# Kernel tuning notes

Measured on AMD Instinct MI355X. Metric: run time of the kernel, lower is better.

Reference implementation:

```python
import jax, jax.numpy as jnp
import numpy as np
from jax import lax

B, T, SDIM, ADIM, HDIM, NH, NBLK, MAXT = 4, 512, 64, 32, 512, 8, 6, 4096
DFF = 4 * HDIM
S = 3 * T  # (num_state_tokens + 1) * context_len
DH = HDIM // NH


def _layernorm(x, g, b, eps=1e-5):
    m = jnp.mean(x, axis=-1, keepdims=True)
    v = jnp.mean((x - m) ** 2, axis=-1, keepdims=True)
    return (x - m) * lax.rsqrt(v + eps) * g + b


def setup_inputs() -> dict:
    key = jax.random.key(0)
    ks = iter(jax.random.split(key, 40))

    def nrm(shape, scale=0.02):
        return jax.random.normal(next(ks), shape, jnp.float32) * scale

    inp = {
        "timesteps": jax.random.randint(next(ks), (B, T), 0, MAXT),
        "state_0": jax.random.normal(next(ks), (B, T, SDIM), jnp.float32),
        "state_1": jax.random.normal(next(ks), (B, T, SDIM), jnp.float32),
        "actions": jax.random.normal(next(ks), (B, T, ADIM), jnp.float32),
        # embeddings / input projections
        "time_emb": nrm((MAXT, HDIM)),
        "Ws": nrm((SDIM, HDIM)), "bs": jnp.zeros((HDIM,), jnp.float32),
        "Wa": nrm((ADIM, HDIM)), "ba": jnp.zeros((HDIM,), jnp.float32),
        # stacked per-block transformer params (leading axis = n_blocks)
        "Wq": nrm((NBLK, HDIM, HDIM)), "bq": jnp.zeros((NBLK, HDIM), jnp.float32),
        "Wk": nrm((NBLK, HDIM, HDIM)), "bk": jnp.zeros((NBLK, HDIM), jnp.float32),
        "Wv": nrm((NBLK, HDIM, HDIM)), "bv": jnp.zeros((NBLK, HDIM), jnp.float32),
        "Wo": nrm((NBLK, HDIM, HDIM)), "bo": jnp.zeros((NBLK, HDIM), jnp.float32),
        "W1": nrm((NBLK, HDIM, DFF)), "b1": jnp.zeros((NBLK, DFF), jnp.float32),
        "W2": nrm((NBLK, DFF, HDIM)), "b2": jnp.zeros((NBLK, HDIM), jnp.float32),
        "ln1_g": jnp.ones((NBLK, HDIM), jnp.float32), "ln1_b": jnp.zeros((NBLK, HDIM), jnp.float32),
        "ln2_g": jnp.ones((NBLK, HDIM), jnp.float32), "ln2_b": jnp.zeros((NBLK, HDIM), jnp.float32),
        # embed layernorm + action head
        "eln_g": jnp.ones((HDIM,), jnp.float32), "eln_b": jnp.zeros((HDIM,), jnp.float32),
        "Wp": nrm((HDIM, ADIM)), "bp": jnp.zeros((ADIM,), jnp.float32),
    }
    return inp


def reference(timesteps, state_0, state_1, actions, time_emb, Ws, bs, Wa, ba,
              Wq, bq, Wk, bk, Wv, bv, Wo, bo, W1, b1, W2, b2,
              ln1_g, ln1_b, ln2_g, ln2_b, eln_g, eln_b, Wp, bp):
    te = time_emb[timesteps]                       # (B, T, H)
    s0 = state_0 @ Ws + bs + te                    # shared state embedding
    s1 = state_1 @ Ws + bs + te
    ae = actions @ Wa + ba + te
    # interleave: (B, T, 3, H) -> (B, 3T, H), token order [s0, s1, a] per timestep
    h = jnp.stack([s0, s1, ae], axis=2).reshape(B, S, HDIM)
    h = _layernorm(h, eln_g, eln_b)

    causal = jnp.tril(jnp.ones((S, S), dtype=bool))
    scale = 1.0 / float(DH) ** 0.5

    def block(x, p):
        wq, bq_, wk, bk_, wv, bv_, wo, bo_, w1, b1_, w2, b2_, g1, be1, g2, be2 = p
        q = (x @ wq + bq_).reshape(B, S, NH, DH)
        k = (x @ wk + bk_).reshape(B, S, NH, DH)
        v = (x @ wv + bv_).reshape(B, S, NH, DH)
        scores = jnp.einsum('bihd,bjhd->bhij', q, k) * scale
        scores = jnp.where(causal, scores, -jnp.inf)
        attn = jax.nn.softmax(scores, axis=-1)
        ctx = jnp.einsum('bhij,bjhd->bihd', attn, v).reshape(B, S, HDIM)
        x = x + (ctx @ wo + bo_)
        x = _layernorm(x, g1, be1)
        mlp = jax.nn.gelu(x @ w1 + b1_, approximate=False) @ w2 + b2_
        x = _layernorm(x + mlp, g2, be2)
        return x, None

    h, _ = lax.scan(block, h,
                    (Wq, bq, Wk, bk, Wv, bv, Wo, bo, W1, b1, W2, b2,
                     ln1_g, ln1_b, ln2_g, ln2_b))

    h = h.reshape(B, T, 3, HDIM)                   # (B, T, num_tokens, H)
    act_in = h[:, :, 1]                            # token index -2 = last state token
    return act_in @ Wp + bp                        # (B, T, act_dim)
```

## Files before the change

kernel.cpp:

```cpp
#include <hip/hip_runtime.h>
#include <hip/hip_bf16.h>
#include <math.h>

#define BB 4
#define TT 512
#define SDIM 64
#define ADIM 32
#define HDIM 512
#define NH 8
#define NBLK 6
#define DFF 2048
#define SS 1536
#define DH 64
#define MS (BB*SS)
#define SZE ((size_t)MS * HDIM)

typedef __attribute__((ext_vector_type(8))) __bf16 bf16x8;
typedef __attribute__((ext_vector_type(4))) float f32x4;

__device__ __forceinline__ __bf16 f2b(float x) { return (__bf16)x; }

__device__ __forceinline__ void gll16(const void* g, void* l) {
    __builtin_amdgcn_global_load_lds(
        (const __attribute__((address_space(1))) unsigned int*)g,
        (__attribute__((address_space(3))) unsigned int*)l, 16, 0, 0);
}

__global__ __launch_bounds__(512) void embed_ln_kernel(
    const int* __restrict__ timesteps,
    const float* __restrict__ state0, const float* __restrict__ state1,
    const float* __restrict__ actions, const float* __restrict__ time_emb,
    const float* __restrict__ Ws, const float* __restrict__ bs,
    const float* __restrict__ Wa, const float* __restrict__ ba,
    const float* __restrict__ eg, const float* __restrict__ eb,
    __bf16* __restrict__ h_bf)
{
    __shared__ float xs[8][64];
    __shared__ float acc_s[8][512];
    __shared__ int tss[8];
    int c = blockIdx.x, t = blockIdx.y, b = blockIdx.z;
    int i0 = c * 8;
    int tid = threadIdx.x;
    int K = (t == 2) ? ADIM : SDIM;
    int ksh = (t == 2) ? 5 : 6;
    const float* W    = (t == 2) ? Wa : Ws;
    const float* bias = (t == 2) ? ba : bs;
    const float* src  = (t == 0) ? state0  + ((size_t)(b*TT + i0)) * SDIM
                      : (t == 1) ? state1  + ((size_t)(b*TT + i0)) * SDIM
                                 : actions + ((size_t)(b*TT + i0)) * ADIM;

    if (tid < 8) tss[tid] = timesteps[b*TT + i0 + tid];
    for (int idx = tid; idx < 8 * K; idx += 512) {
        int r = idx >> ksh, kk = idx & (K - 1);
        xs[r][kk] = src[r * K + kk];
    }
    __syncthreads();

    float acc[8];
    #pragma unroll
    for (int r = 0; r < 8; ++r)
        acc[r] = bias[tid] + time_emb[(size_t)tss[r] * HDIM + tid];
    for (int kk = 0; kk < K; ++kk) {
        float w = W[(size_t)kk * HDIM + tid];
        #pragma unroll
        for (int r = 0; r < 8; ++r) acc[r] += xs[r][kk] * w;
    }
    #pragma unroll
    for (int r = 0; r < 8; ++r) acc_s[r][tid] = acc[r];
    __syncthreads();

    int w = tid >> 6, lane = tid & 63;
    float4 p0 = *(const float4*)&acc_s[w][lane * 8];
    float4 p1 = *(const float4*)&acc_s[w][lane * 8 + 4];
    float v[8] = {p0.x, p0.y, p0.z, p0.w, p1.x, p1.y, p1.z, p1.w};
    float s = 0.f, sq = 0.f;
    #pragma unroll
    for (int u = 0; u < 8; ++u) { s += v[u]; sq += v[u] * v[u]; }
    #pragma unroll
    for (int off = 1; off < 64; off <<= 1) { s += __shfl_xor(s, off); sq += __shfl_xor(sq, off); }
    float mean = s * (1.f / HDIM);
    float var  = sq * (1.f / HDIM) - mean * mean;
    float inv  = rsqrtf(var + 1e-5f);
    float4 g0 = *(const float4*)(eg + lane * 8), g1 = *(const float4*)(eg + lane * 8 + 4);
    float4 b0 = *(const float4*)(eb + lane * 8), b1 = *(const float4*)(eb + lane * 8 + 4);
    float gg[8] = {g0.x, g0.y, g0.z, g0.w, g1.x, g1.y, g1.z, g1.w};
    float bbv[8] = {b0.x, b0.y, b0.z, b0.w, b1.x, b1.y, b1.z, b1.w};
    __bf16 o8[8];
    #pragma unroll
    for (int u = 0; u < 8; ++u) o8[u] = f2b((v[u] - mean) * inv * gg[u] + bbv[u]);
    int row = b * SS + (i0 + w) * 3 + t;
    *(uint4*)(h_bf + (size_t)row * HDIM + lane * 8) = *(uint4*)o8;
}

template<int NP>
__global__ __launch_bounds__(256) void ln_add_kernel(
    __bf16* __restrict__ h_bf, const __bf16* __restrict__ parts,
    const float* __restrict__ g, const float* __restrict__ bvec)
{
    int w = threadIdx.x >> 6, lane = threadIdx.x & 63;
    int row = blockIdx.x * 4 + w;
    size_t base = (size_t)row * HDIM + lane * 8;
    bf16x8 h8 = *(const bf16x8*)(h_bf + base);
    bf16x8 p8[NP];
    #pragma unroll
    for (int p = 0; p < NP; ++p) p8[p] = *(const bf16x8*)(parts + p * SZE + base);
    float v[8], s = 0.f, sq = 0.f;
    #pragma unroll
    for (int u = 0; u < 8; ++u) {
        float acc = (float)h8[u];
        #pragma unroll
        for (int p = 0; p < NP; ++p) acc += (float)p8[p][u];
        v[u] = acc;
        s += acc; sq += acc * acc;
    }
    #pragma unroll
    for (int off = 1; off < 64; off <<= 1) { s += __shfl_xor(s, off); sq += __shfl_xor(sq, off); }
    float mean = s * (1.f / HDIM);
    float var  = sq * (1.f / HDIM) - mean * mean;
    float inv  = rsqrtf(var + 1e-5f);
    float4 g0 = *(const float4*)(g + lane * 8), g1 = *(const float4*)(g + lane * 8 + 4);
    float4 b0 = *(const float4*)(bvec + lane * 8), b1 = *(const float4*)(bvec + lane * 8 + 4);
    float gg[8] = {g0.x, g0.y, g0.z, g0.w, g1.x, g1.y, g1.z, g1.w};
    float bbv[8] = {b0.x, b0.y, b0.z, b0.w, b1.x, b1.y, b1.z, b1.w};
    __bf16 o8[8];
    #pragma unroll
    for (int u = 0; u < 8; ++u) o8[u] = f2b((v[u] - mean) * inv * gg[u] + bbv[u]);
    *(uint4*)(h_bf + base) = *(uint4*)o8;
}

__global__ __launch_bounds__(256) void pack_kernel(
    const float* __restrict__ Wq, const float* __restrict__ Wk,
    const float* __restrict__ Wv, const float* __restrict__ Wo,
    const float* __restrict__ W1, const float* __restrict__ W2,
    const float* __restrict__ bq_, const float* __restrict__ bk_, const float* __restrict__ bv_,
    __bf16* __restrict__ wqkvT, __bf16* __restrict__ woT,
    __bf16* __restrict__ w1T, __bf16* __restrict__ w2T, float* __restrict__ biasq)
{
    int lyr = blockIdx.y;
    const float* wq = Wq + (size_t)lyr * HDIM * HDIM;
    const float* wk = Wk + (size_t)lyr * HDIM * HDIM;
    const float* wv = Wv + (size_t)lyr * HDIM * HDIM;
    const float* wo = Wo + (size_t)lyr * HDIM * HDIM;
    const float* w1 = W1 + (size_t)lyr * HDIM * DFF;
    const float* w2 = W2 + (size_t)lyr * DFF * HDIM;
    const float* bqL = bq_ + (size_t)lyr * HDIM;
    const float* bkL = bk_ + (size_t)lyr * HDIM;
    const float* bvL = bv_ + (size_t)lyr * HDIM;
    wqkvT += (size_t)lyr * 1536 * 512;
    woT   += (size_t)lyr * 512 * 512;
    w1T   += (size_t)lyr * 2048 * 512;
    w2T   += (size_t)lyr * 512 * 2048;
    biasq += (size_t)lyr * 1536;

    int bid = blockIdx.x;
    int tid = threadIdx.x;
    if (bid == 768) {
        for (int i = tid; i < 1536; i += 256)
            biasq[i] = (i < 512) ? bqL[i] : ((i < 1024) ? bkL[i-512] : bvL[i-1024]);
        return;
    }
    __shared__ float Ls[64][65];
    const float* src; __bf16* dst; int K, N, kt, nt;
    if (bid < 192) {
        int sec = bid / 64, t = bid % 64;
        src = (sec == 0) ? wq : (sec == 1) ? wk : wv;
        dst = wqkvT + (size_t)sec * 512 * 512;
        K = 512; N = 512; nt = t >> 3; kt = t & 7;
    } else if (bid < 256) {
        int t = bid - 192; src = wo; dst = woT; K = 512; N = 512; nt = t >> 3; kt = t & 7;
    } else if (bid < 512) {
        int t = bid - 256; src = w1; dst = w1T; K = 512; N = 2048; nt = t >> 3; kt = t & 7;
    } else {
        int t = bid - 512; src = w2; dst = w2T; K = 2048; N = 512; nt = t & 7; kt = t >> 3;
    }
    int k0 = kt * 64, n0 = nt * 64;
    int rr = tid >> 4, cc = (tid & 15) * 4;
    #pragma unroll
    for (int p = 0; p < 4; ++p) {
        float4 v = *(const float4*)(src + (size_t)(k0 + rr + p*16) * N + n0 + cc);
        Ls[rr + p*16][cc] = v.x; Ls[rr + p*16][cc+1] = v.y;
        Ls[rr + p*16][cc+2] = v.z; Ls[rr + p*16][cc+3] = v.w;
    }
    __syncthreads();
    int nn = tid >> 3, kc = (tid & 7) * 8;
    #pragma unroll
    for (int p = 0; p < 2; ++p) {
        __bf16 t8[8];
        #pragma unroll
        for (int t2 = 0; t2 < 8; ++t2) t8[t2] = f2b(Ls[kc + t2][nn + p*32]);
        *(uint4*)(dst + (size_t)(n0 + nn + p*32) * K + k0 + kc) = *(uint4*)t8;
    }
}

template<int MT, bool VTMODE>
__global__ __launch_bounds__(256) void gemm_mfma(
    const __bf16* __restrict__ A, const __bf16* __restrict__ Bt,
    const float* __restrict__ bias, __bf16* __restrict__ C,
    __bf16* __restrict__ VTout,
    int N, int Ksub, int lda, int ldb, int ldc, int gelu, size_t cSplitStride)
{
    constexpr int MI = MT / 32;
    constexpr int SMB0 = 2*MT*64 + 2*128*64;
    constexpr int SMB = (MT*132*2 > SMB0) ? MT*132*2 : SMB0;
    __shared__ __align__(16) char sm[SMB];
    __bf16* As = (__bf16*)sm;
    __bf16* Bs = (__bf16*)(sm + 2*MT*64);
    int tid = threadIdx.x;
    int wave = tid >> 6, lane = tid & 63;
    int l15 = lane & 15, quad = lane >> 4;
    int wy = wave >> 1, wx = wave & 1;
    int m0 = blockIdx.y * MT, n0 = blockIdx.x * 128;
    int zs = blockIdx.z;
    int kbase = zs * Ksub;
    C += (size_t)zs * cSplitStride;

    int srow = lane >> 2;
    int clog = (lane & 3) ^ ((lane >> 3) & 3);
    int pchunk = (quad ^ ((l15 >> 1) & 3)) * 8;

    f32x4 acc[MI][4];
    #pragma unroll
    for (int i = 0; i < MI; ++i)
        #pragma unroll
        for (int j = 0; j < 4; ++j) acc[i][j] = (f32x4){0.f,0.f,0.f,0.f};

    const __bf16* Abase = A  + (size_t)m0 * lda + kbase + clog * 8;
    const __bf16* Bbase = Bt + (size_t)n0 * ldb + kbase + clog * 8;
    int NK = Ksub >> 5;

    #pragma unroll
    for (int q = 0; q < MT/64; ++q) {
        int r0 = (wave * (MT/64) + q) * 16;
        gll16(Abase + (size_t)(r0 + srow) * lda, As + r0*32);
    }
    #pragma unroll
    for (int q = 0; q < 2; ++q) {
        int r0 = (wave * 2 + q) * 16;
        gll16(Bbase + (size_t)(r0 + srow) * ldb, Bs + r0*32);
    }

    for (int kt = 0; kt < NK; ++kt) {
        int buf = kt & 1;
        __syncthreads();
        if (kt + 1 < NK) {
            int k0 = (kt + 1) << 5;
            #pragma unroll
            for (int q = 0; q < MT/64; ++q) {
                int r0 = (wave * (MT/64) + q) * 16;
                gll16(Abase + (size_t)(r0 + srow) * lda + k0, As + ((buf^1)*MT + r0)*32);
            }
            #pragma unroll
            for (int q = 0; q < 2; ++q) {
                int r0 = (wave * 2 + q) * 16;
                gll16(Bbase + (size_t)(r0 + srow) * ldb + k0, Bs + ((buf^1)*128 + r0)*32);
            }
        }
        bf16x8 af[MI], bf[4];
        #pragma unroll
        for (int i = 0; i < MI; ++i)
            af[i] = *(const bf16x8*)&As[(buf*MT + wy*(MT/2) + i*16 + l15)*32 + pchunk];
        #pragma unroll
        for (int j = 0; j < 4; ++j)
            bf[j] = *(const bf16x8*)&Bs[(buf*128 + wx*64 + j*16 + l15)*32 + pchunk];
        #pragma unroll
        for (int i = 0; i < MI; ++i)
            #pragma unroll
            for (int j = 0; j < 4; ++j)
                acc[i][j] = __builtin_amdgcn_mfma_f32_16x16x32_bf16(af[i], bf[j], acc[i][j], 0, 0, 0);
    }

    if (VTMODE && n0 >= 1024) {
        __syncthreads();
        __bf16* T = (__bf16*)sm;
        #pragma unroll
        for (int j = 0; j < 4; ++j) {
            int dl = wx*64 + j*16 + l15;
            float bv = bias[n0 + dl];
            int x31 = dl & 31;
            #pragma unroll
            for (int i = 0; i < MI; ++i) {
                int sc = wy*16 + i*4 + quad;
                int phys = sc ^ x31;
                __bf16 v4[4];
                #pragma unroll
                for (int r = 0; r < 4; ++r) v4[r] = f2b(acc[i][j][r] + bv);
                *(uint2*)(T + dl*128 + phys*4) = *(uint2*)v4;
            }
        }
        __syncthreads();
        int dl = tid >> 1, sh = (tid & 1) * 64;
        int dglob = n0 - 1024 + dl;
        int bb = m0 / SS, srel = m0 - bb*SS;
        __bf16* vb = VTout + ((size_t)(bb*NH + (dglob >> 6)) * 64 + (dglob & 63)) * SS + srel + sh;
        int x31 = dl & 31;
        #pragma unroll
        for (int u = 0; u < 8; ++u) {
            int c0 = (sh >> 2) + u*2;
            uint2 lo = *(const uint2*)(T + dl*128 + ((c0    ) ^ x31)*4);
            uint2 hi = *(const uint2*)(T + dl*128 + ((c0 + 1) ^ x31)*4);
            uint4 o; o.x = lo.x; o.y = lo.y; o.z = hi.x; o.w = hi.y;
            *(uint4*)(vb + u*8) = o;
        }
        return;
    }

    __syncthreads();
    __bf16* T = (__bf16*)sm;
    #pragma unroll
    for (int j = 0; j < 4; ++j) {
        int cl = wx*64 + j*16 + l15;
        float bv = (zs == 0) ? bias[n0 + cl] : 0.f;
        #pragma unroll
        for (int i = 0; i < MI; ++i) {
            #pragma unroll
            for (int r = 0; r < 4; ++r) {
                int rr = wy*(MT/2) + i*16 + quad*4 + r;
                float v = acc[i][j][r] + bv;
                if (gelu) {
                    float u2 = v * (0.7978845608f + 0.0356774081f * v * v);
                    float e  = __builtin_amdgcn_exp2f(u2 * 2.885390082f);
                    v = v * (1.f - __builtin_amdgcn_rcpf(e + 1.f));
                }
                T[rr*132 + cl] = f2b(v);
            }
        }
    }
    __syncthreads();
    constexpr int TPR = 256 / MT;
    constexpr int CPT = 128 / TPR;
    int row = tid / TPR, cp = (tid % TPR) * CPT;
    __bf16* gout = C + (size_t)(m0 + row) * ldc + n0 + cp;
    #pragma unroll
    for (int u = 0; u < CPT/8; ++u) {
        uint2 a = *(const uint2*)&T[row*132 + cp + u*8];
        uint2 b = *(const uint2*)&T[row*132 + cp + u*8 + 4];
        uint4 o; o.x = a.x; o.y = a.y; o.z = b.x; o.w = b.y;
        *(uint4*)(gout + u*8) = o;
    }
}

#define SM_C 0.18033688011112042f

__device__ __forceinline__ unsigned pack2bf(float a, float b)
{
    union { __bf16 h[2]; unsigned u; } t;
    t.h[0] = (__bf16)a; t.h[1] = (__bf16)b;
    return t.u;
}

__device__ __forceinline__ bf16x8 ptrans(const float* p0, const float* p1, int lane)
{
    int l15 = lane & 15, quad = lane >> 4;
    unsigned pk0a = pack2bf(p0[0], p0[1]), pk0b = pack2bf(p0[2], p0[3]);
    unsigned pk1a = pack2bf(p1[0], p1[1]), pk1b = pack2bf(p1[2], p1[3]);
    int sA = l15 + (quad & 1) * 32;
    int sB = sA + 16;
    int hi = quad >> 1;
    unsigned a0A = (unsigned)__shfl((int)pk0a, sA);
    unsigned a1A = (unsigned)__shfl((int)pk1a, sA);
    unsigned b0A = (unsigned)__shfl((int)pk0b, sA);
    unsigned b1A = (unsigned)__shfl((int)pk1b, sA);
    unsigned a0B = (unsigned)__shfl((int)pk0a, sB);
    unsigned a1B = (unsigned)__shfl((int)pk1a, sB);
    unsigned b0B = (unsigned)__shfl((int)pk0b, sB);
    unsigned b1B = (unsigned)__shfl((int)pk1b, sB);
    union { unsigned u[4]; bf16x8 v; } pb;
    pb.u[0] = hi ? a1A : a0A;
    pb.u[1] = hi ? b1A : b0A;
    pb.u[2] = hi ? a1B : a0B;
    pb.u[3] = hi ? b1B : b0B;
    return pb.v;
}

__global__ __launch_bounds__(256, 3) void attn_kernel(
    __bf16* qkc, const __bf16* __restrict__ VT)
{
    __shared__ __align__(16) char smem[32768];

    int x = blockIdx.x;
    int region = x >> 8;
    int j = x & 255;
    int i = j >> 5;
    int hb = j & 31;
    int qt = (region == 0) ? (23 - i) : (region == 1) ? (8 + i) : i;
    int h = hb >> 2, b = hb & 3;

    int tid = threadIdx.x;
    int w = tid >> 6, lane = tid & 63;
    int l15 = lane & 15, quad = lane >> 4;
    int qrow0 = qt * 64 + w * 16;

    const __bf16* qp = qkc + (size_t)(b*SS + qrow0 + l15) * 1024 + h*64 + quad*8;
    bf16x8 qf0 = *(const bf16x8*)qp;
    bf16x8 qf1 = *(const bf16x8*)(qp + 32);

    const __bf16* kgbase = qkc + (size_t)(b*SS) * 1024 + 512 + h*64;
    const __bf16* vgbase = VT + (size_t)(b*NH + h) * 64 * SS;
    int srow8 = lane >> 3;
    int clog  = (lane & 7) ^ ((lane >> 3) & 7);
    int sw0 = ((0*4 + quad) ^ (l15 & 7)) * 8;
    int sw1 = ((1*4 + quad) ^ (l15 & 7)) * 8;

    f32x4 o0 = {0.f,0.f,0.f,0.f}, o1 = o0, o2 = o0, o3 = o0;
    float sm_m = -1e30f, sm_l = 0.f;

    int nkt = qt + 1;

    #pragma unroll
    for (int q = 0; q < 2; ++q) {
        int r0 = (w*2 + q) * 8;
        gll16(kgbase + (size_t)(r0 + srow8) * 1024 + clog*8, (__bf16*)smem + r0*64);
        gll16(vgbase + (size_t)(r0 + srow8) * SS   + clog*8, (__bf16*)(smem + 16384) + r0*64);
    }
    __syncthreads();

    for (int jt = 0; jt < nkt; ++jt) {
        int buf = jt & 1;
        const __bf16* Kb = (const __bf16*)(smem + buf * 8192);
        const __bf16* Vb = (const __bf16*)(smem + 16384 + buf * 8192);
        if (jt + 1 < nkt) {
            int kb2 = (jt + 1) * 64;
            __bf16* Kn = (__bf16*)(smem + (buf ^ 1) * 8192);
            __bf16* Vn = (__bf16*)(smem + 16384 + (buf ^ 1) * 8192);
            #pragma unroll
            for (int q = 0; q < 2; ++q) {
                int r0 = (w*2 + q) * 8;
                gll16(kgbase + (size_t)(kb2 + r0 + srow8) * 1024 + clog*8, Kn + r0*64);
                gll16(vgbase + (size_t)(r0 + srow8) * SS + kb2 + clog*8,   Vn + r0*64);
            }
        }
        int kb = jt * 64;

        f32x4 s[4];
        #pragma unroll
        for (int f = 0; f < 4; ++f) {
            bf16x8 k0 = *(const bf16x8*)(Kb + (16*f + l15)*64 + sw0);
            bf16x8 k1 = *(const bf16x8*)(Kb + (16*f + l15)*64 + sw1);
            f32x4 sf = {0.f,0.f,0.f,0.f};
            sf = __builtin_amdgcn_mfma_f32_16x16x32_bf16(k0, qf0, sf, 0, 0, 0);
            sf = __builtin_amdgcn_mfma_f32_16x16x32_bf16(k1, qf1, sf, 0, 0, 0);
            s[f] = sf;
        }

        if (kb + 63 > qrow0) {
            int qrow = qrow0 + l15;
            #pragma unroll
            for (int f = 0; f < 4; ++f)
                #pragma unroll
                for (int r = 0; r < 4; ++r)
                    if (kb + 16*f + quad*4 + r > qrow) s[f][r] = -1e30f;
        }

        float tf[4];
        #pragma unroll
        for (int f = 0; f < 4; ++f)
            tf[f] = fmaxf(fmaxf(s[f][0], s[f][1]), fmaxf(s[f][2], s[f][3]));
        float tm_lane = fmaxf(fmaxf(tf[0], tf[1]), fmaxf(tf[2], tf[3]));

        if (!__all(tm_lane <= sm_m + 64.f)) {
            float tm = tm_lane;
            tm = fmaxf(tm, __shfl_xor(tm, 16));
            tm = fmaxf(tm, __shfl_xor(tm, 32));
            float mnew = fmaxf(sm_m, tm);
            float alpha = __builtin_amdgcn_exp2f((sm_m - mnew) * SM_C);
            sm_l *= alpha;
            o0 *= alpha; o1 *= alpha; o2 *= alpha; o3 *= alpha;
            sm_m = mnew;
        }

        float negmC = -sm_m * SM_C;
        float pp[4][4];
        float rf[4];
        #pragma unroll
        for (int f = 0; f < 4; ++f) {
            #pragma unroll
            for (int r = 0; r < 4; ++r)
                pp[f][r] = __builtin_amdgcn_exp2f(fmaf(s[f][r], SM_C, negmC));
            rf[f] = (pp[f][0] + pp[f][1]) + (pp[f][2] + pp[f][3]);
        }
        sm_l += (rf[0] + rf[1]) + (rf[2] + rf[3]);

        bf16x8 pb01 = ptrans(pp[0], pp[1], lane);
        bf16x8 pb23 = ptrans(pp[2], pp[3], lane);

        #pragma unroll
        for (int ii = 0; ii < 4; ++ii) {
            bf16x8 va = *(const bf16x8*)(Vb + (16*ii + l15)*64 + sw0);
            bf16x8 vb = *(const bf16x8*)(Vb + (16*ii + l15)*64 + sw1);
            f32x4* op = (ii == 0) ? &o0 : (ii == 1) ? &o1 : (ii == 2) ? &o2 : &o3;
            *op = __builtin_amdgcn_mfma_f32_16x16x32_bf16(va, pb01, *op, 0, 0, 0);
            *op = __builtin_amdgcn_mfma_f32_16x16x32_bf16(vb, pb23, *op, 0, 0, 0);
        }
        __syncthreads();
    }

    sm_l += __shfl_xor(sm_l, 16);
    sm_l += __shfl_xor(sm_l, 32);
    float* otw = (float*)smem + w * 16 * 68;
    float inv = 1.f / sm_l;
    #pragma unroll
    for (int r = 0; r < 4; ++r) {
        otw[l15*68 +  0 + quad*4 + r] = o0[r] * inv;
        otw[l15*68 + 16 + quad*4 + r] = o1[r] * inv;
        otw[l15*68 + 32 + quad*4 + r] = o2[r] * inv;
        otw[l15*68 + 48 + quad*4 + r] = o3[r] * inv;
    }
    asm volatile("s_waitcnt lgkmcnt(0)" ::: "memory");
    int row = lane >> 2, ch = (lane & 3) * 16;
    union { __bf16 hh[16]; uint4 q4[2]; } ob;
    #pragma unroll
    for (int t2 = 0; t2 < 16; ++t2) ob.hh[t2] = f2b(otw[row*68 + ch + t2]);
    __bf16* cp = qkc + (size_t)(b*SS + qrow0 + row) * 1024 + h*64 + ch;
    *(uint4*)cp = ob.q4[0];
    *(uint4*)(cp + 8) = ob.q4[1];
}

__global__ __launch_bounds__(256) void proj_kernel(
    const __bf16* __restrict__ h_bf, const float* __restrict__ Wp,
    const float* __restrict__ bp, float* __restrict__ out)
{
    int rid = blockIdx.x * 8 + (threadIdx.x >> 5);
    int col = threadIdx.x & 31;
    int b = rid / TT, i = rid - b * TT;
    const __bf16* x = h_bf + ((size_t)(b*SS) + 3*i + 1) * HDIM;
    float acc = bp[col];
    for (int k8 = 0; k8 < HDIM/8; ++k8) {
        bf16x8 x8 = *(const bf16x8*)(x + k8*8);
        #pragma unroll
        for (int u = 0; u < 8; ++u)
            acc += (float)x8[u] * Wp[(k8*8 + u) * ADIM + col];
    }
    out[(size_t)rid * ADIM + col] = acc;
}

extern "C" void kernel_launch(void* const* d_in, const int* in_sizes, int n_in,
                              void* d_out, int out_size, void* d_ws, size_t ws_size,
                              hipStream_t stream)
{
    (void)in_sizes; (void)n_in; (void)out_size; (void)ws_size;
    const int*   timesteps = (const int*)  d_in[0];
    const float* state0    = (const float*)d_in[1];
    const float* state1    = (const float*)d_in[2];
    const float* actions   = (const float*)d_in[3];
    const float* time_emb  = (const float*)d_in[4];
    const float* Ws  = (const float*)d_in[5];
    const float* bs  = (const float*)d_in[6];
    const float* Wa  = (const float*)d_in[7];
    const float* ba  = (const float*)d_in[8];
    const float* Wq  = (const float*)d_in[9];
    const float* bq  = (const float*)d_in[10];
    const float* Wk  = (const float*)d_in[11];
    const float* bk  = (const float*)d_in[12];
    const float* Wv  = (const float*)d_in[13];
    const float* bv  = (const float*)d_in[14];
    const float* Wo  = (const float*)d_in[15];
    const float* bo  = (const float*)d_in[16];
    const float* W1  = (const float*)d_in[17];
    const float* b1  = (const float*)d_in[18];
    const float* W2  = (const float*)d_in[19];
    const float* b2  = (const float*)d_in[20];
    const float* ln1g = (const float*)d_in[21];
    const float* ln1b = (const float*)d_in[22];
    const float* ln2g = (const float*)d_in[23];
    const float* ln2b = (const float*)d_in[24];
    const float* elng = (const float*)d_in[25];
    const float* elnb = (const float*)d_in[26];
    const float* Wp   = (const float*)d_in[27];
    const float* bp   = (const float*)d_in[28];
    float* out = (float*)d_out;

    char* p = (char*)d_ws;
    __bf16* h_bf = (__bf16*)p;           p += SZE * 2;
    __bf16* qk   = (__bf16*)p;           p += (size_t)MS * 1024 * 2;
    __bf16* VT   = (__bf16*)p;           p += SZE * 2;
                      p += SZE * 2;
    __bf16* tmp  = (__bf16*)p;           p += SZE * 2 * 2;
    __bf16* wqkvT = (__bf16*)p;          p += (size_t)NBLK * 1536 * 512 * 2;
    __bf16* woT   = (__bf16*)p;          p += (size_t)NBLK * 512 * 512 * 2;
    __bf16* w1T   = (__bf16*)p;          p += (size_t)NBLK * 2048 * 512 * 2;
    __bf16* w2T   = (__bf16*)p;          p += (size_t)NBLK * 512 * 2048 * 2;
    float*  biasq = (float*)p;           p += (size_t)NBLK * 1536 * 4;
    __bf16* hid   = qk;

    embed_ln_kernel<<<dim3(TT/8, 3, BB), 512, 0, stream>>>(timesteps, state0, state1, actions,
                                                           time_emb, Ws, bs, Wa, ba, elng, elnb, h_bf);

    pack_kernel<<<dim3(769, NBLK), 256, 0, stream>>>(Wq, Wk, Wv, Wo, W1, W2, bq, bk, bv,
                                                     wqkvT, woT, w1T, w2T, biasq);

    dim3 gQKV(1536/128, MS/128, 1);
    dim3 gO  (512/128,  MS/64, 2);
    dim3 gF1 (2048/128, MS/128, 1);

    for (int lyr = 0; lyr < NBLK; ++lyr) {
        const __bf16* wqkvT_l = wqkvT + (size_t)lyr * 1536 * 512;
        const __bf16* woT_l   = woT   + (size_t)lyr * 512 * 512;
        const __bf16* w1T_l   = w1T   + (size_t)lyr * 2048 * 512;
        const __bf16* w2T_l   = w2T   + (size_t)lyr * 512 * 2048;
        const float*  biasq_l = biasq + (size_t)lyr * 1536;

        gemm_mfma<128, true><<<gQKV, 256, 0, stream>>>(h_bf, wqkvT_l, biasq_l, qk, VT,
                                                       1536, 512, 512, 512, 1024, 0, 0);
        attn_kernel<<<dim3(768), 256, 0, stream>>>(qk, VT);
        gemm_mfma<64, false><<<gO, 256, 0, stream>>>(qk, woT_l, bo + lyr*HDIM, tmp, nullptr,
                                                     512, 256, 1024, 512, 512, 0, SZE);
        ln_add_kernel<2><<<MS/4, 256, 0, stream>>>(h_bf, tmp,
                                                   ln1g + lyr*HDIM, ln1b + lyr*HDIM);
        gemm_mfma<128, false><<<gF1, 256, 0, stream>>>(h_bf, w1T_l, b1 + lyr*DFF, hid, nullptr,
                                                       2048, 512, 512, 512, 2048, 1, 0);
        gemm_mfma<64, false><<<gO, 256, 0, stream>>>(hid, w2T_l, b2 + lyr*HDIM, tmp, nullptr,
                                                     512, 1024, 2048, 2048, 512, 0, SZE);
        ln_add_kernel<2><<<MS/4, 256, 0, stream>>>(h_bf, tmp,
                                                   ln2g + lyr*HDIM, ln2b + lyr*HDIM);
    }

    proj_kernel<<<(BB*TT)/8, 256, 0, stream>>>(h_bf, Wp, bp, out);
}
```

Baseline: 946.4 us.

## Triple-buffer GEMM loads with explicit vmcnt waits and swizzle epilogue LDS

The GEMM moves from double to triple-buffered LDS staging, issuing loads two k-steps ahead. It replaces __syncthreads with explicit s_waitcnt vmcnt counts plus raw barriers, so outstanding global-to-LDS loads can stay in flight across iterations. The epilogue transpose buffer now uses an XOR swizzle with 16-byte reads instead of padded rows. The attention kernel gets the same explicit-wait prefetch. This costs more LDS per block, which may reduce occupancy, and correctness depends on the hand-computed vmcnt values.

```diff
diff --git a/kernel.cpp b/kernel.cpp
--- a/kernel.cpp
+++ b/kernel.cpp
@@ -24,6 +24,17 @@
     __builtin_amdgcn_global_load_lds(
         (const __attribute__((address_space(1))) unsigned int*)g,
         (__attribute__((address_space(3))) unsigned int*)l, 16, 0, 0);
+}
+
+template<int N> __device__ __forceinline__ void vmwait() {
+    if constexpr (N == 0) asm volatile("s_waitcnt vmcnt(0)" ::: "memory");
+    else if constexpr (N == 3) asm volatile("s_waitcnt vmcnt(3)" ::: "memory");
+    else if constexpr (N == 4) asm volatile("s_waitcnt vmcnt(4)" ::: "memory");
+    else if constexpr (N == 6) asm volatile("s_waitcnt vmcnt(6)" ::: "memory");
+    else if constexpr (N == 8) asm volatile("s_waitcnt vmcnt(8)" ::: "memory");
+}
+__device__ __forceinline__ void lgkm0() {
+    asm volatile("s_waitcnt lgkmcnt(0)" ::: "memory");
 }
 
 __global__ __launch_bounds__(512) void embed_ln_kernel(
@@ -200,11 +211,11 @@
     int N, int Ksub, int lda, int ldb, int ldc, int gelu, size_t cSplitStride)
 {
     constexpr int MI = MT / 32;
-    constexpr int SMB0 = 2*MT*64 + 2*128*64;
-    constexpr int SMB = (MT*132*2 > SMB0) ? MT*132*2 : SMB0;
+    constexpr int LPS = MT/64 + 2;
+    constexpr int SMB = 3*MT*64 + 3*128*64;
     __shared__ __align__(16) char sm[SMB];
     __bf16* As = (__bf16*)sm;
-    __bf16* Bs = (__bf16*)(sm + 2*MT*64);
+    __bf16* Bs = (__bf16*)(sm + 3*MT*64);
     int tid = threadIdx.x;
     int wave = tid >> 6, lane = tid & 63;
     int l15 = lane & 15, quad = lane >> 4;
@@ -228,33 +239,33 @@
     const __bf16* Bbase = Bt + (size_t)n0 * ldb + kbase + clog * 8;
     int NK = Ksub >> 5;
 
-    #pragma unroll
-    for (int q = 0; q < MT/64; ++q) {
-        int r0 = (wave * (MT/64) + q) * 16;
-        gll16(Abase + (size_t)(r0 + srow) * lda, As + r0*32);
-    }
-    #pragma unroll
-    for (int q = 0; q < 2; ++q) {
-        int r0 = (wave * 2 + q) * 16;
-        gll16(Bbase + (size_t)(r0 + srow) * ldb, Bs + r0*32);
-    }
-
+    auto STAGE = [&](int kt2, int b) {
+        int k0 = kt2 << 5;
+        #pragma unroll
+        for (int q = 0; q < MT/64; ++q) {
+            int r0 = (wave * (MT/64) + q) * 16;
+            gll16(Abase + (size_t)(r0 + srow) * lda + k0, As + (b*MT + r0)*32);
+        }
+        #pragma unroll
+        for (int q = 0; q < 2; ++q) {
+            int r0 = (wave * 2 + q) * 16;
+            gll16(Bbase + (size_t)(r0 + srow) * ldb + k0, Bs + (b*128 + r0)*32);
+        }
+    };
+
+    STAGE(0, 0);
+    STAGE(1, 1);
+
+    int buf = 0;
     for (int kt = 0; kt < NK; ++kt) {
-        int buf = kt & 1;
-        __syncthreads();
-        if (kt + 1 < NK) {
-            int k0 = (kt + 1) << 5;
-            #pragma unroll
-            for (int q = 0; q < MT/64; ++q) {
-                int r0 = (wave * (MT/64) + q) * 16;
-                gll16(Abase + (size_t)(r0 + srow) * lda + k0, As + ((buf^1)*MT + r0)*32);
-            }
-            #pragma unroll
-            for (int q = 0; q < 2; ++q) {
-                int r0 = (wave * 2 + q) * 16;
-                gll16(Bbase + (size_t)(r0 + srow) * ldb + k0, Bs + ((buf^1)*128 + r0)*32);
-            }
-        }
+        int bnext = (buf == 2) ? 0 : buf + 1;
+        int b2    = (bnext == 2) ? 0 : bnext + 1;
+        if (kt + 2 < NK) { STAGE(kt + 2, b2); vmwait<2*LPS>(); }
+        else if (kt + 1 < NK) { vmwait<LPS>(); }
+        else { vmwait<0>(); }
+        __builtin_amdgcn_s_barrier();
+        __builtin_amdgcn_sched_barrier(0);
+
         bf16x8 af[MI], bf[4];
         #pragma unroll
         for (int i = 0; i < MI; ++i)
@@ -267,6 +278,10 @@
             #pragma unroll
             for (int j = 0; j < 4; ++j)
                 acc[i][j] = __builtin_amdgcn_mfma_f32_16x16x32_bf16(af[i], bf[j], acc[i][j], 0, 0, 0);
+
+        lgkm0();
+        __builtin_amdgcn_s_barrier();
+        buf = bnext;
     }
 
     if (VTMODE && n0 >= 1024) {
@@ -304,7 +319,6 @@
         return;
     }
 
-    __syncthreads();
     __bf16* T = (__bf16*)sm;
     #pragma unroll
     for (int j = 0; j < 4; ++j) {
@@ -321,7 +335,7 @@
                     float e  = __builtin_amdgcn_exp2f(u2 * 2.885390082f);
                     v = v * (1.f - __builtin_amdgcn_rcpf(e + 1.f));
                 }
-                T[rr*132 + cl] = f2b(v);
+                T[rr*128 + (cl ^ ((rr & 7) << 3))] = f2b(v);
             }
         }
     }
@@ -332,9 +346,8 @@
     __bf16* gout = C + (size_t)(m0 + row) * ldc + n0 + cp;
     #pragma unroll
     for (int u = 0; u < CPT/8; ++u) {
-        uint2 a = *(const uint2*)&T[row*132 + cp + u*8];
-        uint2 b = *(const uint2*)&T[row*132 + cp + u*8 + 4];
-        uint4 o; o.x = a.x; o.y = a.y; o.z = b.x; o.w = b.y;
+        int swc = ((cp >> 3) + u) ^ (row & 7);
+        uint4 o = *(const uint4*)&T[row*128 + swc*8];
         *(uint4*)(gout + u*8) = o;
     }
 }
@@ -406,30 +419,28 @@
 
     int nkt = qt + 1;
 
-    #pragma unroll
-    for (int q = 0; q < 2; ++q) {
-        int r0 = (w*2 + q) * 8;
-        gll16(kgbase + (size_t)(r0 + srow8) * 1024 + clog*8, (__bf16*)smem + r0*64);
-        gll16(vgbase + (size_t)(r0 + srow8) * SS   + clog*8, (__bf16*)(smem + 16384) + r0*64);
-    }
-    __syncthreads();
+    auto STAGEA = [&](int jt2, int bufT) {
+        int kb2 = jt2 * 64;
+        __bf16* Kn = (__bf16*)(smem + bufT * 8192);
+        __bf16* Vn = (__bf16*)(smem + 16384 + bufT * 8192);
+        #pragma unroll
+        for (int q = 0; q < 2; ++q) {
+            int r0 = (w*2 + q) * 8;
+            gll16(kgbase + (size_t)(kb2 + r0 + srow8) * 1024 + clog*8, Kn + r0*64);
+            gll16(vgbase + (size_t)(r0 + srow8) * SS + kb2 + clog*8,   Vn + r0*64);
+        }
+    };
+
+    STAGEA(0, 0);
 
     for (int jt = 0; jt < nkt; ++jt) {
         int buf = jt & 1;
         const __bf16* Kb = (const __bf16*)(smem + buf * 8192);
         const __bf16* Vb = (const __bf16*)(smem + 16384 + buf * 8192);
-        if (jt + 1 < nkt) {
-            int kb2 = (jt + 1) * 64;
-            __bf16* Kn = (__bf16*)(smem + (buf ^ 1) * 8192);
-            __bf16* Vn = (__bf16*)(smem + 16384 + (buf ^ 1) * 8192);
-            #pragma unroll
-            for (int q = 0; q < 2; ++q) {
-                int r0 = (w*2 + q) * 8;
-                gll16(kgbase + (size_t)(kb2 + r0 + srow8) * 1024 + clog*8, Kn + r0*64);
-                gll16(vgbase + (size_t)(r0 + srow8) * SS + kb2 + clog*8,   Vn + r0*64);
-            }
-        }
-        int kb = jt * 64;
+        if (jt + 1 < nkt) { STAGEA(jt + 1, buf ^ 1); vmwait<4>(); }
+        else vmwait<0>();
+        __builtin_amdgcn_s_barrier();
+        __builtin_amdgcn_sched_barrier(0);
 
         f32x4 s[4];
         #pragma unroll
@@ -441,6 +452,7 @@
             sf = __builtin_amdgcn_mfma_f32_16x16x32_bf16(k1, qf1, sf, 0, 0, 0);
             s[f] = sf;
         }
+        int kb = jt * 64;
 
         if (kb + 63 > qrow0) {
             int qrow = qrow0 + l15;
@@ -491,7 +503,9 @@
             *op = __builtin_amdgcn_mfma_f32_16x16x32_bf16(va, pb01, *op, 0, 0, 0);
             *op = __builtin_amdgcn_mfma_f32_16x16x32_bf16(vb, pb23, *op, 0, 0, 0);
         }
-        __syncthreads();
+
+        lgkm0();
+        __builtin_amdgcn_s_barrier();
     }
 
     sm_l += __shfl_xor(sm_l, 16);
@@ -505,7 +519,7 @@
         otw[l15*68 + 32 + quad*4 + r] = o2[r] * inv;
         otw[l15*68 + 48 + quad*4 + r] = o3[r] * inv;
     }
-    asm volatile("s_waitcnt lgkmcnt(0)" ::: "memory");
+    lgkm0();
     int row = lane >> 2, ch = (lane & 3) * 16;
     union { __bf16 hh[16]; uint4 q4[2]; } ob;
     #pragma unroll
```

Result: slower. 1.010 ms (+6.7%).
